# Performance work log

Measured on AMD Instinct MI355X. Metric: run time of the kernel, lower is better.

Reference implementation:

```python
import jax, jax.numpy as jnp
import numpy as np

NUM_HEADS = 10
LN_EPS = 1e-5

def setup_inputs() -> dict:
    key = jax.random.key(0)
    ks = jax.random.split(key, 8)
    B, H, N, D, Dt = 256, 200, 64, 640, 256
    s = 0.02
    return {
        'clicked_news': jax.random.normal(ks[0], (B, H, D), jnp.float32),
        'clicked_topics': jax.random.normal(ks[1], (B, H, Dt), jnp.float32),
        'cand_topics': jax.random.normal(ks[2], (B, N, Dt), jnp.float32),
        'Wq': jax.random.normal(ks[3], (D, Dt), jnp.float32) * s,
        'bq': jnp.zeros((D,), jnp.float32),
        'Wk': jax.random.normal(ks[4], (D, Dt), jnp.float32) * s,
        'bk': jnp.zeros((D,), jnp.float32),
        'Wv': jax.random.normal(ks[5], (D, D), jnp.float32) * s,
        'bv': jnp.zeros((D,), jnp.float32),
        'Wg': jax.random.normal(ks[6], (D, D), jnp.float32) * s,
        'bg': jnp.zeros((D,), jnp.float32),
        'ln_gamma': jnp.ones((D,), jnp.float32),
        'ln_beta': jnp.zeros((D,), jnp.float32),
    }

def reference(clicked_news, clicked_topics, cand_topics, Wq, bq, Wk, bk, Wv, bv, Wg, bg, ln_gamma, ln_beta):
    B, H, D = clicked_news.shape
    N = cand_topics.shape[1]
    nh = NUM_HEADS
    hd = D // nh
    scale = jnp.sqrt(jnp.asarray(D, clicked_news.dtype))

    Qf = cand_topics @ Wq.T + bq            # [B, N, D]
    Kf = clicked_topics @ Wk.T + bk         # [B, H, D]
    # V projection feeds `weighted`, which is dead code w.r.t. outputs; omitted.

    Q = Qf.reshape(B, N, nh, hd)
    K = Kf.reshape(B, H, nh, hd)
    scores = jnp.einsum('bnhd,bmhd->bhnm', Q, K) / scale   # [B, nh, N, H]
    attn = jax.nn.softmax(scores, axis=-1)                 # dropout is identity in eval

    # query weighting: softmax over candidates of ||Q||
    query_weights = jax.nn.softmax(jnp.linalg.norm(Qf, axis=-1), axis=1)   # [B, N]
    agg = (attn.sum(axis=1) * query_weights[:, :, None]).sum(axis=1)       # [B, H]
    attn_weights_agg = jax.nn.softmax(agg, axis=-1)                        # [B, H]

    weighted_clicked = attn_weights_agg[:, :, None] * clicked_news         # [B, H, D]
    gate = jax.nn.sigmoid(weighted_clicked @ Wg.T + bg)
    out = gate * weighted_clicked + (1.0 - gate) * clicked_news

    mu = out.mean(axis=-1, keepdims=True)
    var = out.var(axis=-1, keepdims=True)
    out = (out - mu) / jnp.sqrt(var + LN_EPS) * ln_gamma + ln_beta
    return out, attn_weights_agg
```

## Files before the change

### kernel.cpp

```cpp
#include <hip/hip_runtime.h>
#include <math.h>

#define B_  256
#define H_  200
#define N_  64
#define D_  640
#define DT_ 256
#define NH_ 10
#define HD_ 64
#define MT_ 13

typedef __attribute__((ext_vector_type(8))) short bf16x8;
typedef __attribute__((ext_vector_type(4))) float f32x4;

__device__ __forceinline__ float wave_reduce_sum(float v) {
    #pragma unroll
    for (int m = 32; m > 0; m >>= 1) v += __shfl_xor(v, m);
    return v;
}
__device__ __forceinline__ float wave_reduce_max(float v) {
    #pragma unroll
    for (int m = 32; m > 0; m >>= 1) v = fmaxf(v, __shfl_xor(v, m));
    return v;
}
__device__ __forceinline__ float red16_sum(float v) {
    #pragma unroll
    for (int m = 1; m < 16; m <<= 1) v += __shfl_xor(v, m);
    return v;
}
__device__ __forceinline__ float red16_max(float v) {
    #pragma unroll
    for (int m = 1; m < 16; m <<= 1) v = fmaxf(v, __shfl_xor(v, m));
    return v;
}
__device__ __forceinline__ short f2bf(float x) {
    unsigned u = __float_as_uint(x);
    unsigned r = (u + 0x7fffu + ((u >> 16) & 1u)) >> 16;
    return (short)r;
}
__device__ __forceinline__ float bf2f(short s) {
    return __uint_as_float(((unsigned)(unsigned short)s) << 16);
}
#define SWZ(row, byte) ((byte) ^ (((row) & 7) << 4))
#define WSWZ_S(col, sidx) ((sidx) ^ ((((col) >> 1) & 3) << 3))

__device__ __forceinline__ void gload_lds16(const void* g, void* lds) {
    __builtin_amdgcn_global_load_lds(
        (const __attribute__((address_space(1))) void*)g,
        (__attribute__((address_space(3))) void*)lds, 16, 0, 0);
}

__global__ __launch_bounds__(256) void convert_w(
    const float* __restrict__ src, short* __restrict__ dst, int n)
{
    for (int i = blockIdx.x * 256 + threadIdx.x; i < n; i += gridDim.x * 256)
        dst[i] = f2bf(src[i]);
}

__global__ __launch_bounds__(256) void convert_wg(
    const float* __restrict__ src, short* __restrict__ dst)
{
    for (int i = blockIdx.x * 256 + threadIdx.x; i < D_ * D_; i += gridDim.x * 256) {
        const int col = i / D_, k = i % D_;
        const int kc = k >> 5, kk = k & 31;
        dst[kc * (D_ * 32) + WSWZ_S(col, col * 32 + kk)] = f2bf(src[i]);
    }
}

__global__ __launch_bounds__(512, 2) void proj_mfma(
    const float* __restrict__ X, const short* __restrict__ Wb,
    const float* __restrict__ bias, short* __restrict__ Y)
{
    __shared__ short A_lds[64 * DT_];
    const int t = threadIdx.x;
    const int lane = t & 63, w = t >> 6;
    const int r16 = lane & 15, g = lane >> 4;
    const long row0 = (long)blockIdx.x * 64;

    {
        const int srow = t >> 3, sc = t & 7;
        const float4* src = (const float4*)(X + (row0 + srow) * DT_) + sc;
        float4 sv[8];
        #pragma unroll
        for (int j = 0; j < 8; ++j) sv[j] = src[8 * j];
        #pragma unroll
        for (int j = 0; j < 8; ++j) {
            short4 s;
            s.x = f2bf(sv[j].x); s.y = f2bf(sv[j].y);
            s.z = f2bf(sv[j].z); s.w = f2bf(sv[j].w);
            *(short4*)((char*)A_lds + SWZ(srow, srow * (DT_ * 2) + (sc + 8 * j) * 8)) = s;
        }
    }
    __syncthreads();

    f32x4 acc[5][4];
    #pragma unroll
    for (int ct = 0; ct < 5; ++ct)
        #pragma unroll
        for (int rt = 0; rt < 4; ++rt) acc[ct][rt] = (f32x4){0.f,0.f,0.f,0.f};

    const short* Wbase = Wb + (long)(w * 80 + r16) * DT_ + g * 8;

    bf16x8 aA[4], bA[5], aB[4], bB[5];
    #pragma unroll
    for (int rt = 0; rt < 4; ++rt) {
        const int row = rt * 16 + r16;
        aA[rt] = *(const bf16x8*)((const char*)A_lds + SWZ(row, row * (DT_ * 2) + g * 16));
    }
    #pragma unroll
    for (int ct = 0; ct < 5; ++ct) bA[ct] = *(const bf16x8*)(Wbase + ct * 16 * DT_);

    #pragma unroll
    for (int kc = 0; kc < 8; kc += 2) {
        {
            const int kn = kc + 1;
            #pragma unroll
            for (int rt = 0; rt < 4; ++rt) {
                const int row = rt * 16 + r16;
                aB[rt] = *(const bf16x8*)((const char*)A_lds +
                          SWZ(row, row * (DT_ * 2) + kn * 64 + g * 16));
            }
            #pragma unroll
            for (int ct = 0; ct < 5; ++ct)
                bB[ct] = *(const bf16x8*)(Wbase + ct * 16 * DT_ + kn * 32);
        }
        #pragma unroll
        for (int ct = 0; ct < 5; ++ct)
            #pragma unroll
            for (int rt = 0; rt < 4; ++rt)
                acc[ct][rt] = __builtin_amdgcn_mfma_f32_16x16x32_bf16(
                                  aA[rt], bA[ct], acc[ct][rt], 0, 0, 0);
        {
            const int kn = (kc + 2 < 8) ? kc + 2 : 0;
            #pragma unroll
            for (int rt = 0; rt < 4; ++rt) {
                const int row = rt * 16 + r16;
                aA[rt] = *(const bf16x8*)((const char*)A_lds +
                          SWZ(row, row * (DT_ * 2) + kn * 64 + g * 16));
            }
            #pragma unroll
            for (int ct = 0; ct < 5; ++ct)
                bA[ct] = *(const bf16x8*)(Wbase + ct * 16 * DT_ + kn * 32);
        }
        #pragma unroll
        for (int ct = 0; ct < 5; ++ct)
            #pragma unroll
            for (int rt = 0; rt < 4; ++rt)
                acc[ct][rt] = __builtin_amdgcn_mfma_f32_16x16x32_bf16(
                                  aB[rt], bB[ct], acc[ct][rt], 0, 0, 0);
    }

    #pragma unroll
    for (int ct = 0; ct < 5; ++ct) {
        const int col = w * 80 + ct * 16 + r16;
        const float bv = bias[col];
        #pragma unroll
        for (int rt = 0; rt < 4; ++rt)
            #pragma unroll
            for (int i = 0; i < 4; ++i)
                Y[(row0 + rt * 16 + g * 4 + i) * (long)D_ + col] =
                    f2bf(acc[ct][rt][i] + bv);
    }
}

__global__ __launch_bounds__(512, 2) void attn2(
    const short* __restrict__ Qb, const short* __restrict__ Kb,
    float* __restrict__ aw, float* __restrict__ out_tail)
{
    __shared__ float qn_l[N_];
    __shared__ float qw_l[N_];
    __shared__ float aggp[8][MT_ * 16];
    __shared__ float red2[2];
    const int t = threadIdx.x;
    const int lane = t & 63, w = t >> 6;
    const int wm = w & 3, hh = w >> 2;
    const int r16 = lane & 15, g = lane >> 4;
    const int b = blockIdx.x;

    if (hh == 0) {
        const short* qrow = Qb + ((long)(b * N_ + wm * 16 + r16)) * D_ + g * 160;
        float ss = 0.f;
        #pragma unroll
        for (int j = 0; j < 20; ++j) {
            bf16x8 v = *(const bf16x8*)(qrow + j * 8);
            #pragma unroll
            for (int e = 0; e < 8; ++e) { float f = bf2f(v[e]); ss += f * f; }
        }
        ss += __shfl_xor(ss, 16);
        ss += __shfl_xor(ss, 32);
        if (g == 0) qn_l[wm * 16 + r16] = ss;
    }
    __syncthreads();
    if (w == 0) {
        float v = sqrtf(qn_l[lane]);
        float mx = wave_reduce_max(v);
        float e = __expf(v - mx);
        float s = wave_reduce_sum(e);
        qw_l[lane] = e / s;
    }
    __syncthreads();

    float qwr[4];
    #pragma unroll
    for (int i = 0; i < 4; ++i) qwr[i] = qw_l[wm * 16 + g * 4 + i];

    const float inv_scale = 0.0395284707521047f;
    float aggl[MT_];
    #pragma unroll
    for (int mt = 0; mt < MT_; ++mt) aggl[mt] = 0.f;

    for (int hi = 0; hi < 5; ++hi) {
        const int h = hh * 5 + hi;
        const short* qbase = Qb + ((long)(b * N_ + wm * 16 + r16)) * D_ + h * HD_ + g * 8;
        bf16x8 a0 = *(const bf16x8*)(qbase);
        bf16x8 a1 = *(const bf16x8*)(qbase + 32);
        bf16x8 kb0[MT_], kb1[MT_];
        #pragma unroll
        for (int mt = 0; mt < MT_; ++mt) {
            const short* kbase = Kb + ((long)(b * H_ + mt * 16 + r16)) * D_ + h * HD_ + g * 8;
            kb0[mt] = *(const bf16x8*)(kbase);
            kb1[mt] = *(const bf16x8*)(kbase + 32);
        }
        f32x4 acc[MT_];
        #pragma unroll
        for (int mt = 0; mt < MT_; ++mt) {
            f32x4 z = {0.f,0.f,0.f,0.f};
            z = __builtin_amdgcn_mfma_f32_16x16x32_bf16(a0, kb0[mt], z, 0, 0, 0);
            z = __builtin_amdgcn_mfma_f32_16x16x32_bf16(a1, kb1[mt], z, 0, 0, 0);
            acc[mt] = z;
        }
        const bool tailok = (r16 < 8);
        float mx[4] = {-INFINITY, -INFINITY, -INFINITY, -INFINITY};
        #pragma unroll
        for (int mt = 0; mt < MT_; ++mt) {
            const bool valid = (mt < 12) || tailok;
            #pragma unroll
            for (int i = 0; i < 4; ++i)
                if (valid) mx[i] = fmaxf(mx[i], acc[mt][i]);
        }
        #pragma unroll
        for (int i = 0; i < 4; ++i) mx[i] = red16_max(mx[i]);
        float sum[4] = {0.f, 0.f, 0.f, 0.f};
        #pragma unroll
        for (int mt = 0; mt < MT_; ++mt) {
            const bool valid = (mt < 12) || tailok;
            #pragma unroll
            for (int i = 0; i < 4; ++i) {
                float e = valid ? __expf((acc[mt][i] - mx[i]) * inv_scale) : 0.f;
                acc[mt][i] = e;
                sum[i] += e;
            }
        }
        float fct[4];
        #pragma unroll
        for (int i = 0; i < 4; ++i) fct[i] = qwr[i] / red16_sum(sum[i]);
        #pragma unroll
        for (int mt = 0; mt < MT_; ++mt)
            aggl[mt] += acc[mt][0] * fct[0] + acc[mt][1] * fct[1]
                      + acc[mt][2] * fct[2] + acc[mt][3] * fct[3];
    }
    #pragma unroll
    for (int mt = 0; mt < MT_; ++mt) {
        aggl[mt] += __shfl_xor(aggl[mt], 16);
        aggl[mt] += __shfl_xor(aggl[mt], 32);
    }
    if (g == 0) {
        #pragma unroll
        for (int mt = 0; mt < MT_; ++mt) aggp[w][mt * 16 + r16] = aggl[mt];
    }
    __syncthreads();
    if (t < MT_ * 16) {
        float v = 0.f;
        #pragma unroll
        for (int j = 0; j < 8; ++j) v += aggp[j][t];
        aggp[0][t] = v;
    }
    __syncthreads();
    if (w == 0) {
        float v0 = aggp[0][lane], v1 = aggp[0][lane + 64], v2 = aggp[0][lane + 128];
        const bool has3 = lane < (H_ - 192);
        float v3 = has3 ? aggp[0][lane + 192] : -INFINITY;
        float mx = wave_reduce_max(fmaxf(fmaxf(v0, v1), fmaxf(v2, v3)));
        float s = __expf(v0 - mx) + __expf(v1 - mx) + __expf(v2 - mx)
                + (has3 ? __expf(v3 - mx) : 0.f);
        s = wave_reduce_sum(s);
        if (lane == 0) { red2[0] = mx; red2[1] = s; }
    }
    __syncthreads();
    if (t < H_) {
        float v = __expf(aggp[0][t] - red2[0]) / red2[1];
        aw[b * H_ + t] = v;
        out_tail[b * H_ + t] = v;
    }
}

__global__ __launch_bounds__(512, 2) void out_mfma(
    const float* __restrict__ clicked, const float* __restrict__ aw,
    const short* __restrict__ Wgb, const float* __restrict__ bg,
    const float* __restrict__ gamma, const float* __restrict__ beta,
    float* __restrict__ out)
{
    __shared__ short A_lds[64 * D_];
    __shared__ short W_lds[D_ * 32];
    __shared__ float aw_l[64];
    __shared__ float part[64][8][2];
    __shared__ float mu_l[64], ri_l[64];
    const int t = threadIdx.x;
    const int lane = t & 63, w = t >> 6;
    const int r16 = lane & 15, g = lane >> 4;
    const long row0 = (long)blockIdx.x * 64;

    if (t < 64) aw_l[t] = aw[row0 + t];

    float bgr[5], gmr[5], btr[5];
    #pragma unroll
    for (int ct = 0; ct < 5; ++ct) {
        const int col = w * 80 + ct * 16 + r16;
        bgr[ct] = bg[col]; gmr[ct] = gamma[col]; btr[ct] = beta[col];
    }

    const int arow = t >> 3, aseg = t & 7;
    const float4* Abase = (const float4*)(clicked + (row0 + arow) * D_);

    f32x4 acc[5][4];
    #pragma unroll
    for (int ct = 0; ct < 5; ++ct)
        #pragma unroll
        for (int rt = 0; rt < 4; ++rt) acc[ct][rt] = (f32x4){0.f,0.f,0.f,0.f};

    float4 av = Abase[aseg];

    for (int kc = 0; kc < 20; ++kc) {
        {
            const short* wsrc = Wgb + (long)kc * (D_ * 32);
            #pragma unroll
            for (int j = 0; j < 5; ++j) {
                const int c16 = t + j * 512;
                gload_lds16(wsrc + c16 * 8, (char*)W_lds + c16 * 16);
            }
        }
        {
            short4 s;
            s.x = f2bf(av.x); s.y = f2bf(av.y); s.z = f2bf(av.z); s.w = f2bf(av.w);
            *(short4*)((char*)A_lds +
                SWZ(arow, arow * (D_ * 2) + kc * 64 + aseg * 8)) = s;
        }
        __syncthreads();

        {
            const int kn = (kc + 1 < 20) ? kc + 1 : 0;
            av = Abase[kn * 8 + aseg];
        }

        bf16x8 bb[5];
        #pragma unroll
        for (int ct = 0; ct < 5; ++ct) {
            const int col = w * 80 + ct * 16 + r16;
            bb[ct] = *(const bf16x8*)(W_lds + WSWZ_S(col, col * 32 + g * 8));
        }
        bf16x8 a[4];
        #pragma unroll
        for (int rt = 0; rt < 4; ++rt) {
            const int row = rt * 16 + r16;
            a[rt] = *(const bf16x8*)((const char*)A_lds +
                     SWZ(row, row * (D_ * 2) + kc * 64 + g * 16));
        }
        #pragma unroll
        for (int ct = 0; ct < 5; ++ct)
            #pragma unroll
            for (int rt = 0; rt < 4; ++rt)
                acc[ct][rt] = __builtin_amdgcn_mfma_f32_16x16x32_bf16(
                                  a[rt], bb[ct], acc[ct][rt], 0, 0, 0);
        __syncthreads();
    }

    float psum[4][2], psq[4][2];
    #pragma unroll
    for (int i = 0; i < 4; ++i)
        #pragma unroll
        for (int rt2 = 0; rt2 < 2; ++rt2) { psum[i][rt2] = 0.f; psq[i][rt2] = 0.f; }
    float ps[4][4], pq[4][4];
    #pragma unroll
    for (int rt = 0; rt < 4; ++rt)
        #pragma unroll
        for (int i = 0; i < 4; ++i) { ps[rt][i] = 0.f; pq[rt][i] = 0.f; }

    #pragma unroll
    for (int ct = 0; ct < 5; ++ct) {
        const int col = w * 80 + ct * 16 + r16;
        const float bgv = bgr[ct];
        #pragma unroll
        for (int rt = 0; rt < 4; ++rt)
            #pragma unroll
            for (int i = 0; i < 4; ++i) {
                const int row = rt * 16 + g * 4 + i;
                const float awr = aw_l[row];
                const float cl = bf2f(*(const short*)((const char*)A_lds +
                                   SWZ(row, row * (D_ * 2) + col * 2)));
                const float z  = awr * acc[ct][rt][i] + bgv;
                const float gt = 1.f / (1.f + __expf(-z));
                const float o  = cl * (1.f + gt * (awr - 1.f));
                acc[ct][rt][i] = o;
                ps[rt][i] += o; pq[rt][i] += o * o;
            }
    }
    #pragma unroll
    for (int rt = 0; rt < 4; ++rt)
        #pragma unroll
        for (int i = 0; i < 4; ++i) {
            const float s  = red16_sum(ps[rt][i]);
            const float sq = red16_sum(pq[rt][i]);
            if (r16 == 0) {
                part[rt * 16 + g * 4 + i][w][0] = s;
                part[rt * 16 + g * 4 + i][w][1] = sq;
            }
        }
    __syncthreads();
    if (t < 64) {
        float s = 0.f, q = 0.f;
        #pragma unroll
        for (int j = 0; j < 8; ++j) { s += part[t][j][0]; q += part[t][j][1]; }
        const float m = s * (1.f / D_);
        const float v = q * (1.f / D_) - m * m;
        mu_l[t] = m;
        ri_l[t] = 1.0f / sqrtf(v + 1e-5f);
    }
    __syncthreads();

    #pragma unroll
    for (int ct = 0; ct < 5; ++ct) {
        const int col = w * 80 + ct * 16 + r16;
        const float gmv = gmr[ct], btv = btr[ct];
        #pragma unroll
        for (int rt = 0; rt < 4; ++rt)
            #pragma unroll
            for (int i = 0; i < 4; ++i) {
                const int row = rt * 16 + g * 4 + i;
                out[(row0 + row) * (long)D_ + col] =
                    (acc[ct][rt][i] - mu_l[row]) * ri_l[row] * gmv + btv;
            }
    }
}

extern "C" void kernel_launch(void* const* d_in, const int* in_sizes, int n_in,
                              void* d_out, int out_size, void* d_ws, size_t ws_size,
                              hipStream_t stream) {
    const float* clicked_news   = (const float*)d_in[0];
    const float* clicked_topics = (const float*)d_in[1];
    const float* cand_topics    = (const float*)d_in[2];
    const float* Wq = (const float*)d_in[3];
    const float* bq = (const float*)d_in[4];
    const float* Wk = (const float*)d_in[5];
    const float* bk = (const float*)d_in[6];
    const float* Wg = (const float*)d_in[9];
    const float* bg = (const float*)d_in[10];
    const float* ln_gamma = (const float*)d_in[11];
    const float* ln_beta  = (const float*)d_in[12];

    float* out = (float*)d_out;
    float* ws  = (float*)d_ws;

    float* aw = ws;
    short* sbase = (short*)(ws + (long)B_ * H_);
    short* Qb   = sbase;
    short* Wq_b = Qb + (long)B_ * N_ * D_;
    short* Wg_b = Wq_b + (long)D_ * DT_;
    short* Wk_b = Wg_b + (long)D_ * D_;
    short* Kb = (short*)d_out;
    float* out_tail = out + (long)B_ * H_ * D_;

    convert_w<<<128, 256, 0, stream>>>(Wq, Wq_b, D_ * DT_);
    convert_w<<<128, 256, 0, stream>>>(Wk, Wk_b, D_ * DT_);
    convert_wg<<<256, 256, 0, stream>>>(Wg, Wg_b);

    proj_mfma<<<(B_ * N_) / 64, 512, 0, stream>>>(cand_topics, Wq_b, bq, Qb);
    proj_mfma<<<(B_ * H_) / 64, 512, 0, stream>>>(clicked_topics, Wk_b, bk, Kb);
    attn2<<<B_, 512, 0, stream>>>(Qb, Kb, aw, out_tail);
    out_mfma<<<(B_ * H_) / 64, 512, 0, stream>>>(clicked_news, aw, Wg_b, bg,
                                                 ln_gamma, ln_beta, out);
}
```

Baseline: 316.5 us.

## Double-buffer Wg tiles in out_mfma and move LayerNorm partials to global scratch

The gated-output GEMM kernel now keeps two LDS buffers for the Wg k-slices. The next slice and the next bf16 A chunk are issued before the current MFMAs run, which drops one block barrier per k-iteration and lets global-to-LDS loads overlap compute. To make room in LDS, the per-row LayerNorm partial sums and mean/rstd now live in a per-block global workspace, and attention weights are read straight into registers. This brings global-memory round trips and barrier-ordered global visibility into the epilogue, and grows LDS use to about 160KB per block.

```diff
diff --git a/kernel.cpp b/kernel.cpp
--- a/kernel.cpp
+++ b/kernel.cpp
@@ -298,19 +298,15 @@
     const float* __restrict__ clicked, const float* __restrict__ aw,
     const short* __restrict__ Wgb, const float* __restrict__ bg,
     const float* __restrict__ gamma, const float* __restrict__ beta,
-    float* __restrict__ out)
+    float* __restrict__ out, float* __restrict__ part_g)
 {
     __shared__ short A_lds[64 * D_];
-    __shared__ short W_lds[D_ * 32];
-    __shared__ float aw_l[64];
-    __shared__ float part[64][8][2];
-    __shared__ float mu_l[64], ri_l[64];
+    __shared__ short W_lds[2][D_ * 32];
     const int t = threadIdx.x;
     const int lane = t & 63, w = t >> 6;
     const int r16 = lane & 15, g = lane >> 4;
-    const long row0 = (long)blockIdx.x * 64;
-
-    if (t < 64) aw_l[t] = aw[row0 + t];
+    const int bid = blockIdx.x;
+    const long row0 = (long)bid * 64;
 
     float bgr[5], gmr[5], btr[5];
     #pragma unroll
@@ -320,7 +316,7 @@
     }
 
     const int arow = t >> 3, aseg = t & 7;
-    const float4* Abase = (const float4*)(clicked + (row0 + arow) * D_);
+    const float* Asrc = clicked + (row0 + arow) * D_ + aseg * 4;
 
     f32x4 acc[5][4];
     #pragma unroll
@@ -328,42 +324,53 @@
         #pragma unroll
         for (int rt = 0; rt < 4; ++rt) acc[ct][rt] = (f32x4){0.f,0.f,0.f,0.f};
 
-    float4 av = Abase[aseg];
-
-    for (int kc = 0; kc < 20; ++kc) {
-        {
-            const short* wsrc = Wgb + (long)kc * (D_ * 32);
+    float4 av = *(const float4*)(Asrc);
+    {
+        const short* wsrc = Wgb;
+        #pragma unroll
+        for (int j = 0; j < 5; ++j) {
+            const int u = t + j * 512;
+            gload_lds16(wsrc + u * 8, (char*)W_lds[0] + u * 16);
+        }
+    }
+    {
+        short4 s;
+        s.x = f2bf(av.x); s.y = f2bf(av.y); s.z = f2bf(av.z); s.w = f2bf(av.w);
+        *(short4*)((char*)A_lds + SWZ(arow, arow * (D_ * 2) + 0 * 64 + aseg * 8)) = s;
+    }
+    av = *(const float4*)(Asrc + 32);
+    __syncthreads();
+
+    int cur = 0;
+    for (int k = 0; k < 20; ++k) {
+        const int nxt = cur ^ 1;
+        if (k + 1 < 20) {
+            const short* wsrc = Wgb + (long)(k + 1) * (D_ * 32);
             #pragma unroll
             for (int j = 0; j < 5; ++j) {
-                const int c16 = t + j * 512;
-                gload_lds16(wsrc + c16 * 8, (char*)W_lds + c16 * 16);
-            }
-        }
-        {
+                const int u = t + j * 512;
+                gload_lds16(wsrc + u * 8, (char*)W_lds[nxt] + u * 16);
+            }
             short4 s;
             s.x = f2bf(av.x); s.y = f2bf(av.y); s.z = f2bf(av.z); s.w = f2bf(av.w);
             *(short4*)((char*)A_lds +
-                SWZ(arow, arow * (D_ * 2) + kc * 64 + aseg * 8)) = s;
-        }
-        __syncthreads();
-
-        {
-            const int kn = (kc + 1 < 20) ? kc + 1 : 0;
-            av = Abase[kn * 8 + aseg];
-        }
-
-        bf16x8 bb[5];
-        #pragma unroll
-        for (int ct = 0; ct < 5; ++ct) {
-            const int col = w * 80 + ct * 16 + r16;
-            bb[ct] = *(const bf16x8*)(W_lds + WSWZ_S(col, col * 32 + g * 8));
-        }
+                SWZ(arow, arow * (D_ * 2) + (k + 1) * 64 + aseg * 8)) = s;
+        }
+        if (k + 2 < 20) av = *(const float4*)(Asrc + (k + 2) * 32);
+
         bf16x8 a[4];
         #pragma unroll
         for (int rt = 0; rt < 4; ++rt) {
             const int row = rt * 16 + r16;
             a[rt] = *(const bf16x8*)((const char*)A_lds +
-                     SWZ(row, row * (D_ * 2) + kc * 64 + g * 16));
+                     SWZ(row, row * (D_ * 2) + k * 64 + g * 16));
+        }
+        bf16x8 bb[5];
+        #pragma unroll
+        for (int ct = 0; ct < 5; ++ct) {
+            const int c3 = w * 80 + ct * 16 + r16;
+            bb[ct] = *(const bf16x8*)((const short*)W_lds[cur] +
+                      WSWZ_S(c3, c3 * 32 + g * 8));
         }
         #pragma unroll
         for (int ct = 0; ct < 5; ++ct)
@@ -372,13 +379,16 @@
                 acc[ct][rt] = __builtin_amdgcn_mfma_f32_16x16x32_bf16(
                                   a[rt], bb[ct], acc[ct][rt], 0, 0, 0);
         __syncthreads();
-    }
-
-    float psum[4][2], psq[4][2];
-    #pragma unroll
-    for (int i = 0; i < 4; ++i)
-        #pragma unroll
-        for (int rt2 = 0; rt2 < 2; ++rt2) { psum[i][rt2] = 0.f; psq[i][rt2] = 0.f; }
+        cur = nxt;
+    }
+
+    float awv[4][4];
+    #pragma unroll
+    for (int rt = 0; rt < 4; ++rt)
+        #pragma unroll
+        for (int i = 0; i < 4; ++i)
+            awv[rt][i] = aw[row0 + rt * 16 + g * 4 + i];
+
     float ps[4][4], pq[4][4];
     #pragma unroll
     for (int rt = 0; rt < 4; ++rt)
@@ -388,22 +398,22 @@
     #pragma unroll
     for (int ct = 0; ct < 5; ++ct) {
         const int col = w * 80 + ct * 16 + r16;
-        const float bgv = bgr[ct];
         #pragma unroll
         for (int rt = 0; rt < 4; ++rt)
             #pragma unroll
             for (int i = 0; i < 4; ++i) {
                 const int row = rt * 16 + g * 4 + i;
-                const float awr = aw_l[row];
+                const float awr = awv[rt][i];
                 const float cl = bf2f(*(const short*)((const char*)A_lds +
                                    SWZ(row, row * (D_ * 2) + col * 2)));
-                const float z  = awr * acc[ct][rt][i] + bgv;
+                const float z  = awr * acc[ct][rt][i] + bgr[ct];
                 const float gt = 1.f / (1.f + __expf(-z));
                 const float o  = cl * (1.f + gt * (awr - 1.f));
                 acc[ct][rt][i] = o;
                 ps[rt][i] += o; pq[rt][i] += o * o;
             }
     }
+    float* pg = part_g + (long)bid * 1280;
     #pragma unroll
     for (int rt = 0; rt < 4; ++rt)
         #pragma unroll
@@ -411,35 +421,40 @@
             const float s  = red16_sum(ps[rt][i]);
             const float sq = red16_sum(pq[rt][i]);
             if (r16 == 0) {
-                part[rt * 16 + g * 4 + i][w][0] = s;
-                part[rt * 16 + g * 4 + i][w][1] = sq;
+                const int row = rt * 16 + g * 4 + i;
+                pg[(w * 64 + row) * 2 + 0] = s;
+                pg[(w * 64 + row) * 2 + 1] = sq;
             }
         }
     __syncthreads();
     if (t < 64) {
         float s = 0.f, q = 0.f;
         #pragma unroll
-        for (int j = 0; j < 8; ++j) { s += part[t][j][0]; q += part[t][j][1]; }
+        for (int j = 0; j < 8; ++j) {
+            s += pg[(j * 64 + t) * 2 + 0];
+            q += pg[(j * 64 + t) * 2 + 1];
+        }
         const float m = s * (1.f / D_);
         const float v = q * (1.f / D_) - m * m;
-        mu_l[t] = m;
-        ri_l[t] = 1.0f / sqrtf(v + 1e-5f);
-    }
-    __syncthreads();
-
-    #pragma unroll
-    for (int ct = 0; ct < 5; ++ct) {
-        const int col = w * 80 + ct * 16 + r16;
-        const float gmv = gmr[ct], btv = btr[ct];
-        #pragma unroll
-        for (int rt = 0; rt < 4; ++rt)
-            #pragma unroll
-            for (int i = 0; i < 4; ++i) {
-                const int row = rt * 16 + g * 4 + i;
+        pg[1024 + t * 2 + 0] = m;
+        pg[1024 + t * 2 + 1] = 1.0f / sqrtf(v + 1e-5f);
+    }
+    __syncthreads();
+
+    #pragma unroll
+    for (int rt = 0; rt < 4; ++rt)
+        #pragma unroll
+        for (int i = 0; i < 4; ++i) {
+            const int row = rt * 16 + g * 4 + i;
+            const float mu = pg[1024 + row * 2 + 0];
+            const float ri = pg[1024 + row * 2 + 1];
+            #pragma unroll
+            for (int ct = 0; ct < 5; ++ct) {
+                const int col = w * 80 + ct * 16 + r16;
                 out[(row0 + row) * (long)D_ + col] =
-                    (acc[ct][rt][i] - mu_l[row]) * ri_l[row] * gmv + btv;
-            }
-    }
+                    (acc[ct][rt][i] - mu) * ri * gmr[ct] + btr[ct];
+            }
+        }
 }
 
 extern "C" void kernel_launch(void* const* d_in, const int* in_sizes, int n_in,
@@ -460,8 +475,9 @@
     float* out = (float*)d_out;
     float* ws  = (float*)d_ws;
 
-    float* aw = ws;
-    short* sbase = (short*)(ws + (long)B_ * H_);
+    float* aw     = ws;
+    float* part_g = aw + (long)B_ * H_;
+    short* sbase  = (short*)(part_g + (long)800 * 1280);
     short* Qb   = sbase;
     short* Wq_b = Qb + (long)B_ * N_ * D_;
     short* Wg_b = Wq_b + (long)D_ * DT_;
@@ -477,5 +493,5 @@
     proj_mfma<<<(B_ * H_) / 64, 512, 0, stream>>>(clicked_topics, Wk_b, bk, Kb);
     attn2<<<B_, 512, 0, stream>>>(Qb, Kb, aw, out_tail);
     out_mfma<<<(B_ * H_) / 64, 512, 0, stream>>>(clicked_news, aw, Wg_b, bg,
-                                                 ln_gamma, ln_beta, out);
-}
+                                                 ln_gamma, ln_beta, out, part_g);
+}
```

Result: faster. 299.3 us (-5.4%).

## Restructure gate GEMM to 128-row tiles with fp32 A staged via LDS DMA

Applied to the files above, without the earlier changes.

The output gate GEMM kernel now processes 128 rows per block with 1024 threads (16 waves in a 2x8 grid), doubling reuse of each Wg tile loaded into LDS. The K chunk grows from 32 to 64 with a new XOR-swizzled Wg layout. The fp32 clicked_news tile is loaded straight to LDS with global_load_lds and converted to bf16 at fragment read, instead of a register round trip. The epilogue rereads clicked_news from global instead of keeping a bf16 copy in LDS, which adds global traffic. The conversions are now repeated per wave, and launch bounds of (1024,4) may force heavy register limits.

```diff
diff --git a/kernel.cpp b/kernel.cpp
--- a/kernel.cpp
+++ b/kernel.cpp
@@ -42,7 +42,6 @@
     return __uint_as_float(((unsigned)(unsigned short)s) << 16);
 }
 #define SWZ(row, byte) ((byte) ^ (((row) & 7) << 4))
-#define WSWZ_S(col, sidx) ((sidx) ^ ((((col) >> 1) & 3) << 3))
 
 __device__ __forceinline__ void gload_lds16(const void* g, void* lds) {
     __builtin_amdgcn_global_load_lds(
@@ -62,8 +61,11 @@
 {
     for (int i = blockIdx.x * 256 + threadIdx.x; i < D_ * D_; i += gridDim.x * 256) {
         const int col = i / D_, k = i % D_;
-        const int kc = k >> 5, kk = k & 31;
-        dst[kc * (D_ * 32) + WSWZ_S(col, col * 32 + kk)] = f2bf(src[i]);
+        const int kc = k >> 6, k6 = k & 63;
+        const int ks8 = ((k6 >> 5) << 2) | ((k6 & 31) >> 3);
+        const int elem = k & 7;
+        const int granule = ((col << 3) | ks8) ^ (col & 7);
+        dst[(long)kc * (D_ * 64) + granule * 8 + elem] = f2bf(src[i]);
     }
 }
 
@@ -294,109 +296,99 @@
     }
 }
 
-__global__ __launch_bounds__(512, 2) void out_mfma(
+__global__ __launch_bounds__(1024, 4) void out_mfma(
     const float* __restrict__ clicked, const float* __restrict__ aw,
     const short* __restrict__ Wgb, const float* __restrict__ bg,
     const float* __restrict__ gamma, const float* __restrict__ beta,
     float* __restrict__ out)
 {
-    __shared__ short A_lds[64 * D_];
-    __shared__ short W_lds[D_ * 32];
-    __shared__ float aw_l[64];
-    __shared__ float part[64][8][2];
-    __shared__ float mu_l[64], ri_l[64];
+    __shared__ short W_lds[D_ * 64];
+    __shared__ float A_f[128 * 64];
     const int t = threadIdx.x;
     const int lane = t & 63, w = t >> 6;
+    const int wm = w >> 3, wn = w & 7;
     const int r16 = lane & 15, g = lane >> 4;
-    const long row0 = (long)blockIdx.x * 64;
-
-    if (t < 64) aw_l[t] = aw[row0 + t];
-
-    float bgr[5], gmr[5], btr[5];
+    const int bid = blockIdx.x;
+    const long row0 = (long)bid * 128;
+
+    f32x4 acc[5][4];
+    #pragma unroll
+    for (int ct = 0; ct < 5; ++ct)
+        #pragma unroll
+        for (int rt = 0; rt < 4; ++rt) acc[ct][rt] = (f32x4){0.f,0.f,0.f,0.f};
+
+    const int a_row0 = t >> 4,        a_j0 = t & 15;
+    const int a_row1 = (t >> 4) + 64, a_j1 = t & 15;
+    const float* Ag0 = clicked + (row0 + a_row0) * (long)D_ + ((a_j0 ^ (a_row0 & 7)) << 2);
+    const float* Ag1 = clicked + (row0 + a_row1) * (long)D_ + ((a_j1 ^ (a_row1 & 7)) << 2);
+
+    for (int k = 0; k < 10; ++k) {
+        {
+            const short* wsrc = Wgb + (long)k * (D_ * 64);
+            #pragma unroll
+            for (int j = 0; j < 5; ++j) {
+                const int u = t + j * 1024;
+                gload_lds16(wsrc + u * 8, (char*)W_lds + u * 16);
+            }
+        }
+        gload_lds16(Ag0 + k * 64, (char*)A_f + t * 16);
+        gload_lds16(Ag1 + k * 64, (char*)A_f + (t + 1024) * 16);
+        __syncthreads();
+
+        #pragma unroll
+        for (int kk = 0; kk < 2; ++kk) {
+            bf16x8 a[4];
+            #pragma unroll
+            for (int rt = 0; rt < 4; ++rt) {
+                const int row = wm * 64 + rt * 16 + r16;
+                const int j0 = kk * 8 + g * 2;
+                float4 f0 = *(const float4*)((const char*)A_f +
+                             row * 256 + ((j0 ^ (row & 7)) << 4));
+                float4 f1 = *(const float4*)((const char*)A_f +
+                             row * 256 + (((j0 + 1) ^ (row & 7)) << 4));
+                bf16x8 av;
+                av[0] = f2bf(f0.x); av[1] = f2bf(f0.y); av[2] = f2bf(f0.z); av[3] = f2bf(f0.w);
+                av[4] = f2bf(f1.x); av[5] = f2bf(f1.y); av[6] = f2bf(f1.z); av[7] = f2bf(f1.w);
+                a[rt] = av;
+            }
+            #pragma unroll
+            for (int ct = 0; ct < 5; ++ct) {
+                const int col = wn * 80 + ct * 16 + r16;
+                const int granule = ((col << 3) | (kk * 4 + g)) ^ (col & 7);
+                bf16x8 bb = *(const bf16x8*)((const char*)W_lds + granule * 16);
+                #pragma unroll
+                for (int rt = 0; rt < 4; ++rt)
+                    acc[ct][rt] = __builtin_amdgcn_mfma_f32_16x16x32_bf16(
+                                      a[rt], bb, acc[ct][rt], 0, 0, 0);
+            }
+        }
+        __syncthreads();
+    }
+
+    float awv[4][4];
+    #pragma unroll
+    for (int rt = 0; rt < 4; ++rt)
+        #pragma unroll
+        for (int i = 0; i < 4; ++i)
+            awv[rt][i] = aw[row0 + wm * 64 + rt * 16 + g * 4 + i];
+
+    float ps[4][4], pq[4][4];
+    #pragma unroll
+    for (int rt = 0; rt < 4; ++rt)
+        #pragma unroll
+        for (int i = 0; i < 4; ++i) { ps[rt][i] = 0.f; pq[rt][i] = 0.f; }
+
     #pragma unroll
     for (int ct = 0; ct < 5; ++ct) {
-        const int col = w * 80 + ct * 16 + r16;
-        bgr[ct] = bg[col]; gmr[ct] = gamma[col]; btr[ct] = beta[col];
-    }
-
-    const int arow = t >> 3, aseg = t & 7;
-    const float4* Abase = (const float4*)(clicked + (row0 + arow) * D_);
-
-    f32x4 acc[5][4];
-    #pragma unroll
-    for (int ct = 0; ct < 5; ++ct)
-        #pragma unroll
-        for (int rt = 0; rt < 4; ++rt) acc[ct][rt] = (f32x4){0.f,0.f,0.f,0.f};
-
-    float4 av = Abase[aseg];
-
-    for (int kc = 0; kc < 20; ++kc) {
-        {
-            const short* wsrc = Wgb + (long)kc * (D_ * 32);
-            #pragma unroll
-            for (int j = 0; j < 5; ++j) {
-                const int c16 = t + j * 512;
-                gload_lds16(wsrc + c16 * 8, (char*)W_lds + c16 * 16);
-            }
-        }
-        {
-            short4 s;
-            s.x = f2bf(av.x); s.y = f2bf(av.y); s.z = f2bf(av.z); s.w = f2bf(av.w);
-            *(short4*)((char*)A_lds +
-                SWZ(arow, arow * (D_ * 2) + kc * 64 + aseg * 8)) = s;
-        }
-        __syncthreads();
-
-        {
-            const int kn = (kc + 1 < 20) ? kc + 1 : 0;
-            av = Abase[kn * 8 + aseg];
-        }
-
-        bf16x8 bb[5];
-        #pragma unroll
-        for (int ct = 0; ct < 5; ++ct) {
-            const int col = w * 80 + ct * 16 + r16;
-            bb[ct] = *(const bf16x8*)(W_lds + WSWZ_S(col, col * 32 + g * 8));
-        }
-        bf16x8 a[4];
-        #pragma unroll
-        for (int rt = 0; rt < 4; ++rt) {
-            const int row = rt * 16 + r16;
-            a[rt] = *(const bf16x8*)((const char*)A_lds +
-                     SWZ(row, row * (D_ * 2) + kc * 64 + g * 16));
-        }
-        #pragma unroll
-        for (int ct = 0; ct < 5; ++ct)
-            #pragma unroll
-            for (int rt = 0; rt < 4; ++rt)
-                acc[ct][rt] = __builtin_amdgcn_mfma_f32_16x16x32_bf16(
-                                  a[rt], bb[ct], acc[ct][rt], 0, 0, 0);
-        __syncthreads();
-    }
-
-    float psum[4][2], psq[4][2];
-    #pragma unroll
-    for (int i = 0; i < 4; ++i)
-        #pragma unroll
-        for (int rt2 = 0; rt2 < 2; ++rt2) { psum[i][rt2] = 0.f; psq[i][rt2] = 0.f; }
-    float ps[4][4], pq[4][4];
-    #pragma unroll
-    for (int rt = 0; rt < 4; ++rt)
-        #pragma unroll
-        for (int i = 0; i < 4; ++i) { ps[rt][i] = 0.f; pq[rt][i] = 0.f; }
-
-    #pragma unroll
-    for (int ct = 0; ct < 5; ++ct) {
-        const int col = w * 80 + ct * 16 + r16;
-        const float bgv = bgr[ct];
+        const int col = wn * 80 + ct * 16 + r16;
+        const float bgv = bg[col];
         #pragma unroll
         for (int rt = 0; rt < 4; ++rt)
             #pragma unroll
             for (int i = 0; i < 4; ++i) {
-                const int row = rt * 16 + g * 4 + i;
-                const float awr = aw_l[row];
-                const float cl = bf2f(*(const short*)((const char*)A_lds +
-                                   SWZ(row, row * (D_ * 2) + col * 2)));
+                const int row = wm * 64 + rt * 16 + g * 4 + i;
+                const float awr = awv[rt][i];
+                const float cl = clicked[(row0 + row) * (long)D_ + col];
                 const float z  = awr * acc[ct][rt][i] + bgv;
                 const float gt = 1.f / (1.f + __expf(-z));
                 const float o  = cl * (1.f + gt * (awr - 1.f));
@@ -404,6 +396,7 @@
                 ps[rt][i] += o; pq[rt][i] += o * o;
             }
     }
+    float* scr = (float*)W_lds;
     #pragma unroll
     for (int rt = 0; rt < 4; ++rt)
         #pragma unroll
@@ -411,35 +404,40 @@
             const float s  = red16_sum(ps[rt][i]);
             const float sq = red16_sum(pq[rt][i]);
             if (r16 == 0) {
-                part[rt * 16 + g * 4 + i][w][0] = s;
-                part[rt * 16 + g * 4 + i][w][1] = sq;
-            }
-        }
-    __syncthreads();
-    if (t < 64) {
+                const int row = wm * 64 + rt * 16 + g * 4 + i;
+                scr[(row * 8 + wn) * 2 + 0] = s;
+                scr[(row * 8 + wn) * 2 + 1] = sq;
+            }
+        }
+    __syncthreads();
+    if (t < 128) {
         float s = 0.f, q = 0.f;
         #pragma unroll
-        for (int j = 0; j < 8; ++j) { s += part[t][j][0]; q += part[t][j][1]; }
+        for (int j = 0; j < 8; ++j) {
+            s += scr[(t * 8 + j) * 2 + 0];
+            q += scr[(t * 8 + j) * 2 + 1];
+        }
         const float m = s * (1.f / D_);
         const float v = q * (1.f / D_) - m * m;
-        mu_l[t] = m;
-        ri_l[t] = 1.0f / sqrtf(v + 1e-5f);
-    }
-    __syncthreads();
-
-    #pragma unroll
-    for (int ct = 0; ct < 5; ++ct) {
-        const int col = w * 80 + ct * 16 + r16;
-        const float gmv = gmr[ct], btv = btr[ct];
-        #pragma unroll
-        for (int rt = 0; rt < 4; ++rt)
-            #pragma unroll
-            for (int i = 0; i < 4; ++i) {
-                const int row = rt * 16 + g * 4 + i;
+        scr[2048 + t * 2 + 0] = m;
+        scr[2048 + t * 2 + 1] = 1.0f / sqrtf(v + 1e-5f);
+    }
+    __syncthreads();
+
+    #pragma unroll
+    for (int rt = 0; rt < 4; ++rt)
+        #pragma unroll
+        for (int i = 0; i < 4; ++i) {
+            const int row = wm * 64 + rt * 16 + g * 4 + i;
+            const float mu = scr[2048 + row * 2 + 0];
+            const float ri = scr[2048 + row * 2 + 1];
+            #pragma unroll
+            for (int ct = 0; ct < 5; ++ct) {
+                const int col = wn * 80 + ct * 16 + r16;
                 out[(row0 + row) * (long)D_ + col] =
-                    (acc[ct][rt][i] - mu_l[row]) * ri_l[row] * gmv + btv;
-            }
-    }
+                    (acc[ct][rt][i] - mu) * ri * gamma[col] + beta[col];
+            }
+        }
 }
 
 extern "C" void kernel_launch(void* const* d_in, const int* in_sizes, int n_in,
@@ -460,8 +458,8 @@
     float* out = (float*)d_out;
     float* ws  = (float*)d_ws;
 
-    float* aw = ws;
-    short* sbase = (short*)(ws + (long)B_ * H_);
+    float* aw     = ws;
+    short* sbase  = (short*)(aw + (long)B_ * H_);
     short* Qb   = sbase;
     short* Wq_b = Qb + (long)B_ * N_ * D_;
     short* Wg_b = Wq_b + (long)D_ * DT_;
@@ -476,6 +474,6 @@
     proj_mfma<<<(B_ * N_) / 64, 512, 0, stream>>>(cand_topics, Wq_b, bq, Qb);
     proj_mfma<<<(B_ * H_) / 64, 512, 0, stream>>>(clicked_topics, Wk_b, bk, Kb);
     attn2<<<B_, 512, 0, stream>>>(Qb, Kb, aw, out_tail);
-    out_mfma<<<(B_ * H_) / 64, 512, 0, stream>>>(clicked_news, aw, Wg_b, bg,
-                                                 ln_gamma, ln_beta, out);
-}
+    out_mfma<<<(B_ * H_) / 128, 1024, 0, stream>>>(clicked_news, aw, Wg_b, bg,
+                                                   ln_gamma, ln_beta, out);
+}
```

Result: slower. 488.7 us (+54.4%).
